# Kernel optimization log

Measured on AMD Instinct MI355X. Metric: run time of the kernel, lower is better.

The kernel has to match this reference:

```python
import jax, jax.numpy as jnp
import numpy as np

N_BINS = 15


def setup_inputs() -> dict:
    key = jax.random.key(0)
    k1, k2 = jax.random.split(key)
    N, C = 2_000_000, 100
    logits = jax.random.normal(k1, (N, C), dtype=jnp.float32)
    labels = jax.random.randint(k2, (N,), 0, C, dtype=jnp.int64)
    temperature = jnp.ones((1,), dtype=jnp.float32)
    return {"logits": logits, "labels": labels, "temperature": temperature}


def reference(logits, labels, temperature):
    # logits: [N, C], labels: [N] int, temperature: [1]
    softmaxes = jax.nn.softmax(logits / temperature[0], axis=1)
    confidences = jnp.max(softmaxes, axis=1)            # [N]
    predictions = jnp.argmax(softmaxes, axis=1)          # [N]
    accuracies = (predictions == labels).astype(softmaxes.dtype)

    # bin b covers (b/n_bins, (b+1)/n_bins]; ceil(conf*n)-1 gives exactly that
    # half-open-on-left binning (conf > 0 always holds after softmax).
    bin_idx = jnp.clip(
        jnp.ceil(confidences * N_BINS).astype(jnp.int32) - 1, 0, N_BINS - 1
    )

    ones = jnp.ones_like(confidences)
    counts = jax.ops.segment_sum(ones, bin_idx, num_segments=N_BINS)
    sum_conf = jax.ops.segment_sum(confidences, bin_idx, num_segments=N_BINS)
    sum_acc = jax.ops.segment_sum(accuracies, bin_idx, num_segments=N_BINS)

    n_total = confidences.shape[0]
    prop_in_bin = counts / n_total
    safe_counts = jnp.maximum(counts, 1.0)
    avg_conf = sum_conf / safe_counts
    avg_acc = sum_acc / safe_counts
    gap = jnp.where(counts > 0, jnp.abs(avg_conf - avg_acc), 0.0)
    ece = jnp.sum(gap * prop_in_bin)
    return ece.reshape(1)
```

## Files before the change

### kernel.cpp

```cpp
#include <hip/hip_runtime.h>
#include <math.h>

#define NBINS 15

typedef float f32x4 __attribute__((ext_vector_type(4)));

__global__ void ece_init(float* accum) {
    int t = threadIdx.x;
    if (t < 48) accum[t] = 0.0f;
}

__device__ __forceinline__ void process4(
    const f32x4* __restrict__ logits4,
    const int* __restrict__ labels,
    long long base, int g, int c, bool has2, float k, int N,
    float& cnt, float& sconf, float& sacc)
{
    long long row = base + g;
    const bool valid = (row < (long long)N);
    const long long r = valid ? row : (long long)(N - 1);
    const f32x4* rowp4 = logits4 + (size_t)r * 25;

    f32x4 a = __builtin_nontemporal_load(rowp4 + c);
    f32x4 b = (f32x4){-INFINITY, -INFINITY, -INFINITY, -INFINITY};
    if (has2) b = __builtin_nontemporal_load(rowp4 + 16 + c);

    a *= k;
    b *= k;

    float lm = a.x; int lidx = 4 * c;
    if (a.y > lm) { lm = a.y; lidx = 4 * c + 1; }
    if (a.z > lm) { lm = a.z; lidx = 4 * c + 2; }
    if (a.w > lm) { lm = a.w; lidx = 4 * c + 3; }
    if (b.x > lm) { lm = b.x; lidx = 64 + 4 * c; }
    if (b.y > lm) { lm = b.y; lidx = 64 + 4 * c + 1; }
    if (b.z > lm) { lm = b.z; lidx = 64 + 4 * c + 2; }
    if (b.w > lm) { lm = b.w; lidx = 64 + 4 * c + 3; }

    float s0 = __builtin_amdgcn_exp2f(a.x - lm) + __builtin_amdgcn_exp2f(a.y - lm)
             + __builtin_amdgcn_exp2f(a.z - lm) + __builtin_amdgcn_exp2f(a.w - lm)
             + __builtin_amdgcn_exp2f(b.x - lm) + __builtin_amdgcn_exp2f(b.y - lm)
             + __builtin_amdgcn_exp2f(b.z - lm) + __builtin_amdgcn_exp2f(b.w - lm);

    float gm = lm;
    gm = fmaxf(gm, __shfl_xor(gm, 1));
    gm = fmaxf(gm, __shfl_xor(gm, 2));
    gm = fmaxf(gm, __shfl_xor(gm, 4));
    gm = fmaxf(gm, __shfl_xor(gm, 8));

    int cand = (lm == gm) ? lidx : 0x7fffffff;
    cand = min(cand, __shfl_xor(cand, 1));
    cand = min(cand, __shfl_xor(cand, 2));
    cand = min(cand, __shfl_xor(cand, 4));
    cand = min(cand, __shfl_xor(cand, 8));

    float s = s0 * __builtin_amdgcn_exp2f(lm - gm);
    s += __shfl_xor(s, 1);
    s += __shfl_xor(s, 2);
    s += __shfl_xor(s, 4);
    s += __shfl_xor(s, 8);

    float conf = 1.0f / s;
    int   lbl  = labels[r];
    float acc  = (cand == lbl) ? 1.0f : 0.0f;
    int bin = (int)ceilf(conf * 15.0f) - 1;
    bin = bin < 0 ? 0 : (bin > 14 ? 14 : bin);

    if (valid && c == bin) {
        cnt   += 1.0f;
        sconf += conf;
        sacc  += acc;
    }
}

__global__ __launch_bounds__(256) void ece_main(
    const float* __restrict__ logits,
    const int* __restrict__ labels,
    const float* __restrict__ temp,
    float* __restrict__ accum,
    int N)
{
    const float k = (1.0f / temp[0]) * 1.44269504088896340736f;
    const int tid  = threadIdx.x;
    const int lane = tid & 63;
    const int c    = lane & 15;
    const int g    = lane >> 4;
    const int wavesPerBlock = blockDim.x >> 6;
    const long long waveId     = (long long)blockIdx.x * wavesPerBlock + (tid >> 6);
    const long long totalWaves = (long long)gridDim.x * wavesPerBlock;

    const f32x4* logits4 = reinterpret_cast<const f32x4*>(logits);
    float cnt = 0.f, sconf = 0.f, sacc = 0.f;
    const bool has2 = (c < 9);

    for (long long base = waveId * 8; base < (long long)N; base += totalWaves * 8) {
        process4(logits4, labels, base,     g, c, has2, k, N, cnt, sconf, sacc);
        process4(logits4, labels, base + 4, g, c, has2, k, N, cnt, sconf, sacc);
    }

    __shared__ float sh[48];
    if (tid < 48) sh[tid] = 0.0f;
    __syncthreads();
    if (c < NBINS) {
        atomicAdd(&sh[c],      cnt);
        atomicAdd(&sh[16 + c], sconf);
        atomicAdd(&sh[32 + c], sacc);
    }
    __syncthreads();
    if (tid < 48) {
        atomicAdd(&accum[tid], sh[tid]);
    }
}

__global__ void ece_final(const float* __restrict__ accum, float* __restrict__ out, float nTotal) {
    if (threadIdx.x == 0) {
        float e = 0.0f;
        for (int b = 0; b < NBINS; b++) {
            float cntv = accum[b];
            float sc   = accum[16 + b];
            float sa   = accum[32 + b];
            float safe = fmaxf(cntv, 1.0f);
            float gap  = (cntv > 0.0f) ? fabsf(sc / safe - sa / safe) : 0.0f;
            e += gap * (cntv / nTotal);
        }
        out[0] = e;
    }
}

extern "C" void kernel_launch(void* const* d_in, const int* in_sizes, int n_in,
                              void* d_out, int out_size, void* d_ws, size_t ws_size,
                              hipStream_t stream) {
    const float* logits = (const float*)d_in[0];
    const int*   labels = (const int*)d_in[1];
    const float* temp   = (const float*)d_in[2];
    float* accum = (float*)d_ws;
    const int N = in_sizes[1];

    ece_init<<<1, 64, 0, stream>>>(accum);
    ece_main<<<2048, 256, 0, stream>>>(logits, labels, temp, accum, N);
    ece_final<<<1, 64, 0, stream>>>(accum, (float*)d_out, (float)N);
}
```

Baseline: 174.1 us.

## Batch four row-group loads per iteration and fold ECE finalization into last block

The main loop now processes 16 rows per wave per iteration, issuing all logits and label loads for four row groups before any compute, so more memory requests are in flight. Nontemporal loads are replaced with regular loads. The final ECE reduction moves into the last-finishing block via an atomic ticket counter, and a trivial copy kernel remains to write the output. This costs more registers for the batched loads, and the ticket path adds a fence and atomic per block.

```diff
diff --git a/kernel.cpp b/kernel.cpp
--- a/kernel.cpp
+++ b/kernel.cpp
@@ -7,70 +7,7 @@
 
 __global__ void ece_init(float* accum) {
     int t = threadIdx.x;
-    if (t < 48) accum[t] = 0.0f;
-}
-
-__device__ __forceinline__ void process4(
-    const f32x4* __restrict__ logits4,
-    const int* __restrict__ labels,
-    long long base, int g, int c, bool has2, float k, int N,
-    float& cnt, float& sconf, float& sacc)
-{
-    long long row = base + g;
-    const bool valid = (row < (long long)N);
-    const long long r = valid ? row : (long long)(N - 1);
-    const f32x4* rowp4 = logits4 + (size_t)r * 25;
-
-    f32x4 a = __builtin_nontemporal_load(rowp4 + c);
-    f32x4 b = (f32x4){-INFINITY, -INFINITY, -INFINITY, -INFINITY};
-    if (has2) b = __builtin_nontemporal_load(rowp4 + 16 + c);
-
-    a *= k;
-    b *= k;
-
-    float lm = a.x; int lidx = 4 * c;
-    if (a.y > lm) { lm = a.y; lidx = 4 * c + 1; }
-    if (a.z > lm) { lm = a.z; lidx = 4 * c + 2; }
-    if (a.w > lm) { lm = a.w; lidx = 4 * c + 3; }
-    if (b.x > lm) { lm = b.x; lidx = 64 + 4 * c; }
-    if (b.y > lm) { lm = b.y; lidx = 64 + 4 * c + 1; }
-    if (b.z > lm) { lm = b.z; lidx = 64 + 4 * c + 2; }
-    if (b.w > lm) { lm = b.w; lidx = 64 + 4 * c + 3; }
-
-    float s0 = __builtin_amdgcn_exp2f(a.x - lm) + __builtin_amdgcn_exp2f(a.y - lm)
-             + __builtin_amdgcn_exp2f(a.z - lm) + __builtin_amdgcn_exp2f(a.w - lm)
-             + __builtin_amdgcn_exp2f(b.x - lm) + __builtin_amdgcn_exp2f(b.y - lm)
-             + __builtin_amdgcn_exp2f(b.z - lm) + __builtin_amdgcn_exp2f(b.w - lm);
-
-    float gm = lm;
-    gm = fmaxf(gm, __shfl_xor(gm, 1));
-    gm = fmaxf(gm, __shfl_xor(gm, 2));
-    gm = fmaxf(gm, __shfl_xor(gm, 4));
-    gm = fmaxf(gm, __shfl_xor(gm, 8));
-
-    int cand = (lm == gm) ? lidx : 0x7fffffff;
-    cand = min(cand, __shfl_xor(cand, 1));
-    cand = min(cand, __shfl_xor(cand, 2));
-    cand = min(cand, __shfl_xor(cand, 4));
-    cand = min(cand, __shfl_xor(cand, 8));
-
-    float s = s0 * __builtin_amdgcn_exp2f(lm - gm);
-    s += __shfl_xor(s, 1);
-    s += __shfl_xor(s, 2);
-    s += __shfl_xor(s, 4);
-    s += __shfl_xor(s, 8);
-
-    float conf = 1.0f / s;
-    int   lbl  = labels[r];
-    float acc  = (cand == lbl) ? 1.0f : 0.0f;
-    int bin = (int)ceilf(conf * 15.0f) - 1;
-    bin = bin < 0 ? 0 : (bin > 14 ? 14 : bin);
-
-    if (valid && c == bin) {
-        cnt   += 1.0f;
-        sconf += conf;
-        sacc  += acc;
-    }
+    if (t < 64) accum[t] = 0.0f;
 }
 
 __global__ __launch_bounds__(256) void ece_main(
@@ -78,7 +15,7 @@
     const int* __restrict__ labels,
     const float* __restrict__ temp,
     float* __restrict__ accum,
-    int N)
+    int N, float nTotal)
 {
     const float k = (1.0f / temp[0]) * 1.44269504088896340736f;
     const int tid  = threadIdx.x;
@@ -93,9 +30,69 @@
     float cnt = 0.f, sconf = 0.f, sacc = 0.f;
     const bool has2 = (c < 9);
 
-    for (long long base = waveId * 8; base < (long long)N; base += totalWaves * 8) {
-        process4(logits4, labels, base,     g, c, has2, k, N, cnt, sconf, sacc);
-        process4(logits4, labels, base + 4, g, c, has2, k, N, cnt, sconf, sacc);
+    for (long long base = waveId * 16; base < (long long)N; base += totalWaves * 16) {
+        f32x4 a[4], b[4];
+        int   lbl[4];
+        bool  valid[4];
+#pragma unroll
+        for (int j = 0; j < 4; j++) {
+            long long row = base + 4 * j + g;
+            valid[j] = (row < (long long)N);
+            long long r = valid[j] ? row : (long long)(N - 1);
+            const f32x4* rowp4 = logits4 + (size_t)r * 25;
+            a[j] = rowp4[c];
+            b[j] = has2 ? rowp4[16 + c]
+                        : (f32x4){-INFINITY, -INFINITY, -INFINITY, -INFINITY};
+            lbl[j] = labels[r];
+        }
+#pragma unroll
+        for (int j = 0; j < 4; j++) {
+            f32x4 av = a[j] * k;
+            f32x4 bv = b[j] * k;
+
+            float lm = av.x; int lidx = 4 * c;
+            if (av.y > lm) { lm = av.y; lidx = 4 * c + 1; }
+            if (av.z > lm) { lm = av.z; lidx = 4 * c + 2; }
+            if (av.w > lm) { lm = av.w; lidx = 4 * c + 3; }
+            if (bv.x > lm) { lm = bv.x; lidx = 64 + 4 * c; }
+            if (bv.y > lm) { lm = bv.y; lidx = 64 + 4 * c + 1; }
+            if (bv.z > lm) { lm = bv.z; lidx = 64 + 4 * c + 2; }
+            if (bv.w > lm) { lm = bv.w; lidx = 64 + 4 * c + 3; }
+
+            float s0 = __builtin_amdgcn_exp2f(av.x - lm) + __builtin_amdgcn_exp2f(av.y - lm)
+                     + __builtin_amdgcn_exp2f(av.z - lm) + __builtin_amdgcn_exp2f(av.w - lm)
+                     + __builtin_amdgcn_exp2f(bv.x - lm) + __builtin_amdgcn_exp2f(bv.y - lm)
+                     + __builtin_amdgcn_exp2f(bv.z - lm) + __builtin_amdgcn_exp2f(bv.w - lm);
+
+            float gm = lm;
+            gm = fmaxf(gm, __shfl_xor(gm, 1));
+            gm = fmaxf(gm, __shfl_xor(gm, 2));
+            gm = fmaxf(gm, __shfl_xor(gm, 4));
+            gm = fmaxf(gm, __shfl_xor(gm, 8));
+
+            int cand = (lm == gm) ? lidx : 0x7fffffff;
+            cand = min(cand, __shfl_xor(cand, 1));
+            cand = min(cand, __shfl_xor(cand, 2));
+            cand = min(cand, __shfl_xor(cand, 4));
+            cand = min(cand, __shfl_xor(cand, 8));
+
+            float s = s0 * __builtin_amdgcn_exp2f(lm - gm);
+            s += __shfl_xor(s, 1);
+            s += __shfl_xor(s, 2);
+            s += __shfl_xor(s, 4);
+            s += __shfl_xor(s, 8);
+
+            float conf = 1.0f / s;
+            float acc  = (cand == lbl[j]) ? 1.0f : 0.0f;
+            int bin = (int)ceilf(conf * 15.0f) - 1;
+            bin = bin < 0 ? 0 : (bin > 14 ? 14 : bin);
+
+            if (valid[j] && c == bin) {
+                cnt   += 1.0f;
+                sconf += conf;
+                sacc  += acc;
+            }
+        }
     }
 
     __shared__ float sh[48];
@@ -110,21 +107,39 @@
     if (tid < 48) {
         atomicAdd(&accum[tid], sh[tid]);
     }
+
+    __shared__ int amLast;
+    if (tid == 0) {
+        __threadfence();
+        unsigned old = atomicAdd(reinterpret_cast<unsigned*>(accum + 48), 1u);
+        amLast = (old == (unsigned)(gridDim.x - 1));
+    }
+    __syncthreads();
+    if (amLast) {
+        float e = 0.0f;
+        if (tid < NBINS) {
+            float cv = atomicAdd(&accum[tid],      0.0f);
+            float sc = atomicAdd(&accum[16 + tid], 0.0f);
+            float sa = atomicAdd(&accum[32 + tid], 0.0f);
+            float safe = fmaxf(cv, 1.0f);
+            float gap  = (cv > 0.0f) ? fabsf(sc / safe - sa / safe) : 0.0f;
+            e = gap * (cv / nTotal);
+        }
+        if (tid < 16) {
+            e += __shfl_xor(e, 1);
+            e += __shfl_xor(e, 2);
+            e += __shfl_xor(e, 4);
+            e += __shfl_xor(e, 8);
+        }
+        if (tid == 0) {
+            float* out = accum + 56;
+            out[0] = e;
+        }
+    }
 }
 
-__global__ void ece_final(const float* __restrict__ accum, float* __restrict__ out, float nTotal) {
-    if (threadIdx.x == 0) {
-        float e = 0.0f;
-        for (int b = 0; b < NBINS; b++) {
-            float cntv = accum[b];
-            float sc   = accum[16 + b];
-            float sa   = accum[32 + b];
-            float safe = fmaxf(cntv, 1.0f);
-            float gap  = (cntv > 0.0f) ? fabsf(sc / safe - sa / safe) : 0.0f;
-            e += gap * (cntv / nTotal);
-        }
-        out[0] = e;
-    }
+__global__ void ece_out(const float* __restrict__ accum, float* __restrict__ out) {
+    if (threadIdx.x == 0) out[0] = accum[56];
 }
 
 extern "C" void kernel_launch(void* const* d_in, const int* in_sizes, int n_in,
@@ -137,6 +152,6 @@
     const int N = in_sizes[1];
 
     ece_init<<<1, 64, 0, stream>>>(accum);
-    ece_main<<<2048, 256, 0, stream>>>(logits, labels, temp, accum, N);
-    ece_final<<<1, 64, 0, stream>>>(accum, (float*)d_out, (float)N);
+    ece_main<<<2048, 256, 0, stream>>>(logits, labels, temp, accum, N, (float)N);
+    ece_out<<<1, 64, 0, stream>>>(accum, (float*)d_out);
 }
```

Result: slower. 241.3 us (+38.5%).
